# Optimization experiments

Hardware: AMD Instinct MI355X
Metric: run time of the kernel (lower is better)

Reference implementation:

```python
import jax, jax.numpy as jnp
from jax import lax
import numpy as np

OUT_CH = 64
K = 7
STRIDE = 2
PAD = 3
HIDDEN = 128
MAX_IN = 3


def setup_inputs() -> dict:
    key = jax.random.key(0)
    k1, k2, k3, k4, k5 = jax.random.split(key, 5)
    B, C, H, W = 32, MAX_IN, 224, 224
    x = jax.random.normal(k1, (B, C, H, W), dtype=jnp.float32)
    channel_mask = jnp.ones((B, C), dtype=jnp.float32)
    # kernel_generator params: Linear(3,128) -> ReLU -> Linear(128, 64*3*7*7)
    W1 = jax.random.normal(k2, (MAX_IN, HIDDEN), dtype=jnp.float32) / np.sqrt(MAX_IN)
    b1 = jnp.zeros((HIDDEN,), dtype=jnp.float32)
    out_dim = OUT_CH * MAX_IN * K * K
    W2 = jax.random.normal(k3, (HIDDEN, out_dim), dtype=jnp.float32) / np.sqrt(HIDDEN)
    b2 = jnp.zeros((out_dim,), dtype=jnp.float32)
    return {"x": x, "channel_mask": channel_mask, "W1": W1, "b1": b1, "W2": W2, "b2": b2}


def reference(x, channel_mask, W1, b1, W2, b2):
    B, C, H, W = x.shape
    # MLP kernel generator: [B, 3] -> [B, out*C*K*K]
    h = jax.nn.relu(channel_mask @ W1 + b1)
    weights = (h @ W2 + b2).reshape(B * OUT_CH, C, K, K)
    # grouped conv, groups = B (per-sample dynamic kernels)
    out = lax.conv_general_dilated(
        x.reshape(1, B * C, H, W),
        weights,
        window_strides=(STRIDE, STRIDE),
        padding=[(PAD, PAD), (PAD, PAD)],
        feature_group_count=B,
        dimension_numbers=("NCHW", "OIHW", "NCHW"),
    )
    return out.reshape(B, OUT_CH, out.shape[2], out.shape[3])
```

## Files before the change

### kernel.cpp

```cpp
#include <hip/hip_runtime.h>
#include <hip/hip_bf16.h>

#define OUT_CH 64
#define KSZ 7
#define STRIDE 2
#define PAD 3
#define HIDDEN 128
#define MAX_IN 3
#define B_SZ 32
#define H_IN 224
#define W_IN 224
#define H_OUT 112
#define W_OUT 112
#define WPB 147
#define OUT_DIM (OUT_CH * WPB)
#define SEGS 21
#define SEGP 24
#define WQ_PER_B (OUT_CH * SEGP * 8)
#define XRW 120
#define XSROWS 24
#define WGEN_BLOCKS 384
#define XPREP_BLOCKS 10080

typedef __attribute__((ext_vector_type(8))) short short8;
typedef __attribute__((ext_vector_type(4))) float floatx4;

__global__ void prep_kernel(const float* __restrict__ x,
                            const float* __restrict__ mask,
                            const float* __restrict__ W1,
                            const float* __restrict__ b1,
                            const float* __restrict__ W2,
                            const float* __restrict__ b2,
                            __hip_bfloat16* __restrict__ wq,
                            unsigned int* __restrict__ xbf,
                            unsigned int* __restrict__ zpad) {
    __shared__ float hs[4][HIDDEN];
    const int tid = threadIdx.x;
    const int bid = blockIdx.x;

    if (bid < WGEN_BLOCKS) {
        const int gb    = bid / 48;
        const int chunk = bid - gb * 48;
        const int b0 = gb * 4;

        for (int i = tid; i < 4 * HIDDEN; i += 256) {
            int q = i >> 7;
            int j = i & (HIDDEN - 1);
            float a = b1[j];
#pragma unroll
            for (int c = 0; c < MAX_IN; ++c)
                a += mask[(b0 + q) * MAX_IN + c] * W1[c * HIDDEN + j];
            hs[q][j] = fmaxf(a, 0.0f);
        }
        __syncthreads();

        const int op = chunk * 256 + tid;
        const int oc  = op / 192;
        const int r   = op - oc * 192;
        const int mi  = r >> 5;
        const int lg  = (r >> 3) & 3;
        const int e   = r & 7;
        const int seg = 4 * mi + 2 * (lg >> 1) + (e >> 2);
        const int tap = 4 * (lg & 1) + (e & 3);

        float acc[4] = {0.0f, 0.0f, 0.0f, 0.0f};
        if (seg < SEGS && tap < KSZ) {
            int o = oc * WPB + seg * KSZ + tap;
            float bias = b2[o];
#pragma unroll
            for (int q = 0; q < 4; ++q) acc[q] = bias;
            const float* w2p = W2 + o;
#pragma unroll 8
            for (int j = 0; j < HIDDEN; ++j) {
                float w = w2p[(size_t)j * OUT_DIM];
#pragma unroll
                for (int q = 0; q < 4; ++q) acc[q] += hs[q][j] * w;
            }
        }
#pragma unroll
        for (int q = 0; q < 4; ++q)
            wq[(size_t)(b0 + q) * WQ_PER_B + op] = __float2bfloat16(acc[q]);
    } else {
        const int xbid = bid - WGEN_BLOCKS;
        int s = xbid * 256 + tid;
        int r = s / XRW;
        int uw = s - r * XRW;
        const float* xr = x + (size_t)r * W_IN;
        int iw0 = 2 * uw - 3;
        float f0 = ((unsigned)iw0 < (unsigned)W_IN) ? xr[iw0] : 0.0f;
        float f1 = ((unsigned)(iw0 + 1) < (unsigned)W_IN) ? xr[iw0 + 1] : 0.0f;
        unsigned int lo = __bfloat16_as_ushort(__float2bfloat16(f0));
        unsigned int hi = __bfloat16_as_ushort(__float2bfloat16(f1));
        xbf[s] = lo | (hi << 16);
        if (xbid == 0 && tid < XRW) zpad[tid] = 0;
    }
}

__global__ void __launch_bounds__(256, 6)
conv_kernel(const unsigned int* __restrict__ xbf,
            const unsigned int* __restrict__ zpad,
            const __hip_bfloat16* __restrict__ wq,
            float* __restrict__ out) {
    __shared__ unsigned int xs[XSROWS * XRW];

    const int xblk = blockIdx.x;
    const int oh = (xblk & 7) * 14 + (xblk >> 3);
    const int b  = blockIdx.y;
    const int tid = threadIdx.x;
    const int w  = tid >> 6;
    const int l  = tid & 63;
    const int lr = l & 15;
    const int lg = l >> 4;

    const unsigned short* wqb = (const unsigned short*)wq
        + ((size_t)b * OUT_CH + w * 16 + lr) * (SEGP * 8);
    short8 afr[6];
#pragma unroll
    for (int mi = 0; mi < 6; ++mi)
        afr[mi] = *(const short8*)(wqb + mi * 32 + lg * 8);

    const int halfl = l / 30;
    const int lc    = l - 30 * halfl;
#pragma unroll
    for (int i = 0; i < 3; ++i) {
        int d   = w + 4 * i;
        int seg = 2 * d + halfl;
        const unsigned int* src = zpad;
        if (seg < SEGS) {
            int c  = seg / KSZ;
            int kh = seg - c * KSZ;
            int ih = oh * STRIDE + kh - PAD;
            if ((unsigned)ih < (unsigned)H_IN)
                src = xbf + ((size_t)(b * MAX_IN + c) * H_IN + ih) * XRW;
        }
        if (l < 60)
            __builtin_amdgcn_global_load_lds(
                (const __attribute__((address_space(1))) unsigned int*)(src + lc * 4),
                (__attribute__((address_space(3))) unsigned int*)(xs + d * 240),
                16, 0, 0);
    }
    __syncthreads();

    const int col = lr + 2 * (lg & 1);
    int ra[6], rb[6];
#pragma unroll
    for (int mi = 0; mi < 6; ++mi) {
        int sa = 4 * mi + 2 * (lg >> 1);
        int sb = sa + 1;
        ra[mi] = (sa < SEGS ? sa : 0) * XRW + col;
        rb[mi] = (sb < SEGS ? sb : 0) * XRW + col;
    }

#pragma unroll
    for (int t = 0; t < 7; ++t) {
        const int tb = t * 16;
        floatx4 acc = {0.0f, 0.0f, 0.0f, 0.0f};
#pragma unroll
        for (int mi = 0; mi < 6; ++mi) {
            union { short8 s; unsigned int u[4]; } bu;
            const unsigned int* pa = xs + ra[mi] + tb;
            const unsigned int* pb = xs + rb[mi] + tb;
            bu.u[0] = pa[0];
            bu.u[1] = pa[1];
            bu.u[2] = pb[0];
            bu.u[3] = pb[1];
            acc = __builtin_amdgcn_mfma_f32_16x16x32_bf16(afr[mi], bu.s, acc, 0, 0, 0);
        }
        const int ow = tb + lr;
        float* op = out + (((size_t)b * OUT_CH + w * 16 + lg * 4) * H_OUT + oh) * W_OUT + ow;
#pragma unroll
        for (int r = 0; r < 4; ++r)
            op[(size_t)r * H_OUT * W_OUT] = acc[r];
    }
}

extern "C" void kernel_launch(void* const* d_in, const int* in_sizes, int n_in,
                              void* d_out, int out_size, void* d_ws, size_t ws_size,
                              hipStream_t stream) {
    const float* x    = (const float*)d_in[0];
    const float* mask = (const float*)d_in[1];
    const float* W1   = (const float*)d_in[2];
    const float* b1   = (const float*)d_in[3];
    const float* W2   = (const float*)d_in[4];
    const float* b2   = (const float*)d_in[5];
    float* out = (float*)d_out;

    __hip_bfloat16* wq  = (__hip_bfloat16*)d_ws;
    unsigned int* xbf   = (unsigned int*)((char*)d_ws + 786432);
    unsigned int* zpad  = (unsigned int*)((char*)d_ws + 786432 + (size_t)B_SZ * MAX_IN * H_IN * XRW * 4);

    prep_kernel<<<dim3(WGEN_BLOCKS + XPREP_BLOCKS), dim3(256), 0, stream>>>(
        x, mask, W1, b1, W2, b2, wq, xbf, zpad);
    conv_kernel<<<dim3(112, B_SZ), dim3(256), 0, stream>>>(xbf, zpad, wq, out);
}
```

Measured before the change: 37.78 us.

## Have each conv wave compute two output-channel tiles over a split range of width tiles

The four waves are remapped so each computes two 16-channel output tiles over half of the seven width tiles, instead of one tile over all seven. Each LDS B-fragment read now feeds two MFMAs, roughly halving LDS traffic per MFMA, and the row-offset tables are replaced by one shared base address. In exchange each wave holds twice as many weight fragments in registers, and the occupancy hint drops from 6 to 4 blocks. The width split is uneven (4 tiles vs 3), so waves in a block may finish at different times.

```diff
diff --git a/kernel.cpp b/kernel.cpp
--- a/kernel.cpp
+++ b/kernel.cpp
@@ -96,7 +96,7 @@
     }
 }
 
-__global__ void __launch_bounds__(256, 6)
+__global__ void __launch_bounds__(256, 4)
 conv_kernel(const unsigned int* __restrict__ xbf,
             const unsigned int* __restrict__ zpad,
             const __hip_bfloat16* __restrict__ wq,
@@ -111,13 +111,23 @@
     const int l  = tid & 63;
     const int lr = l & 15;
     const int lg = l >> 4;
-
-    const unsigned short* wqb = (const unsigned short*)wq
-        + ((size_t)b * OUT_CH + w * 16 + lr) * (SEGP * 8);
-    short8 afr[6];
-#pragma unroll
-    for (int mi = 0; mi < 6; ++mi)
-        afr[mi] = *(const short8*)(wqb + mi * 32 + lg * 8);
+    const int ocp  = w >> 1;
+    const int tset = w & 1;
+
+    short8 afr[2][6];
+#pragma unroll
+    for (int q = 0; q < 2; ++q) {
+        const unsigned short* wqb = (const unsigned short*)wq
+            + ((size_t)b * OUT_CH + (2 * ocp + q) * 16 + lr) * (SEGP * 8);
+#pragma unroll
+        for (int mi = 0; mi < 6; ++mi)
+            afr[q][mi] = *(const short8*)(wqb + mi * 32 + lg * 8);
+    }
+#pragma unroll
+    for (int q = 0; q < 2; ++q)
+#pragma unroll
+        for (int mi = 0; mi < 6; ++mi)
+            asm volatile("" : "+v"(afr[q][mi]));
 
     const int halfl = l / 30;
     const int lc    = l - 30 * halfl;
@@ -142,35 +152,33 @@
     __syncthreads();
 
     const int col = lr + 2 * (lg & 1);
-    int ra[6], rb[6];
-#pragma unroll
-    for (int mi = 0; mi < 6; ++mi) {
-        int sa = 4 * mi + 2 * (lg >> 1);
-        int sb = sa + 1;
-        ra[mi] = (sa < SEGS ? sa : 0) * XRW + col;
-        rb[mi] = (sb < SEGS ? sb : 0) * XRW + col;
-    }
-
-#pragma unroll
-    for (int t = 0; t < 7; ++t) {
+    const int rbase = 2 * (lg >> 1) * XRW + col;
+
+    const int t0 = tset ? 4 : 0;
+    const int t1 = tset ? 7 : 4;
+    for (int t = t0; t < t1; ++t) {
         const int tb = t * 16;
-        floatx4 acc = {0.0f, 0.0f, 0.0f, 0.0f};
+        floatx4 acc0 = {0.0f, 0.0f, 0.0f, 0.0f};
+        floatx4 acc1 = {0.0f, 0.0f, 0.0f, 0.0f};
 #pragma unroll
         for (int mi = 0; mi < 6; ++mi) {
+            const unsigned int* pa = xs + (4 * mi) * XRW + rbase + tb;
             union { short8 s; unsigned int u[4]; } bu;
-            const unsigned int* pa = xs + ra[mi] + tb;
-            const unsigned int* pb = xs + rb[mi] + tb;
             bu.u[0] = pa[0];
             bu.u[1] = pa[1];
-            bu.u[2] = pb[0];
-            bu.u[3] = pb[1];
-            acc = __builtin_amdgcn_mfma_f32_16x16x32_bf16(afr[mi], bu.s, acc, 0, 0, 0);
+            bu.u[2] = pa[XRW];
+            bu.u[3] = pa[XRW + 1];
+            acc0 = __builtin_amdgcn_mfma_f32_16x16x32_bf16(afr[0][mi], bu.s, acc0, 0, 0, 0);
+            acc1 = __builtin_amdgcn_mfma_f32_16x16x32_bf16(afr[1][mi], bu.s, acc1, 0, 0, 0);
         }
         const int ow = tb + lr;
-        float* op = out + (((size_t)b * OUT_CH + w * 16 + lg * 4) * H_OUT + oh) * W_OUT + ow;
-#pragma unroll
-        for (int r = 0; r < 4; ++r)
-            op[(size_t)r * H_OUT * W_OUT] = acc[r];
+        float* op0 = out + (((size_t)b * OUT_CH + (2 * ocp) * 16 + lg * 4) * H_OUT + oh) * W_OUT + ow;
+        float* op1 = op0 + (size_t)16 * H_OUT * W_OUT;
+#pragma unroll
+        for (int r = 0; r < 4; ++r) {
+            op0[(size_t)r * H_OUT * W_OUT] = acc0[r];
+            op1[(size_t)r * H_OUT * W_OUT] = acc1[r];
+        }
     }
 }
 
```

Result: slower. 48.08 us (+27.3%).

## Compute two output rows per conv block to reuse overlapping input rows

Applied to the files above, without the earlier changes.

Each conv block now produces two adjacent output rows, loading 9 input rows per channel (27 plus a zero row) into shared memory instead of 7 per channel per output row. Overlapping rows are shared between the two outputs, and the per-batch weight fragments are loaded once for twice the work. This cuts redundant global-to-LDS input traffic and weight loads. In exchange the grid is halved to 56x32 blocks and each block uses more LDS, which lowers parallelism.

```diff
diff --git a/kernel.cpp b/kernel.cpp
--- a/kernel.cpp
+++ b/kernel.cpp
@@ -18,7 +18,8 @@
 #define SEGP 24
 #define WQ_PER_B (OUT_CH * SEGP * 8)
 #define XRW 120
-#define XSROWS 24
+#define XSROWS 28
+#define ZROW 27
 #define WGEN_BLOCKS 384
 #define XPREP_BLOCKS 10080
 
@@ -104,7 +105,8 @@
     __shared__ unsigned int xs[XSROWS * XRW];
 
     const int xblk = blockIdx.x;
-    const int oh = (xblk & 7) * 14 + (xblk >> 3);
+    const int ohp = (xblk & 7) * 7 + (xblk >> 3);
+    const int oh0 = ohp * 2;
     const int b  = blockIdx.y;
     const int tid = threadIdx.x;
     const int w  = tid >> 6;
@@ -122,14 +124,15 @@
     const int halfl = l / 30;
     const int lc    = l - 30 * halfl;
 #pragma unroll
-    for (int i = 0; i < 3; ++i) {
-        int d   = w + 4 * i;
-        int seg = 2 * d + halfl;
+    for (int i = 0; i < 4; ++i) {
+        int d = w + 4 * i;
+        if (d >= XSROWS / 2) break;
+        int row = 2 * d + halfl;
         const unsigned int* src = zpad;
-        if (seg < SEGS) {
-            int c  = seg / KSZ;
-            int kh = seg - c * KSZ;
-            int ih = oh * STRIDE + kh - PAD;
+        if (row < 27) {
+            int c = row / 9;
+            int j = row - c * 9;
+            int ih = 2 * oh0 + j - PAD;
             if ((unsigned)ih < (unsigned)H_IN)
                 src = xbf + ((size_t)(b * MAX_IN + c) * H_IN + ih) * XRW;
         }
@@ -142,35 +145,49 @@
     __syncthreads();
 
     const int col = lr + 2 * (lg & 1);
-    int ra[6], rb[6];
-#pragma unroll
-    for (int mi = 0; mi < 6; ++mi) {
-        int sa = 4 * mi + 2 * (lg >> 1);
-        int sb = sa + 1;
-        ra[mi] = (sa < SEGS ? sa : 0) * XRW + col;
-        rb[mi] = (sb < SEGS ? sb : 0) * XRW + col;
-    }
-
-#pragma unroll
-    for (int t = 0; t < 7; ++t) {
-        const int tb = t * 16;
-        floatx4 acc = {0.0f, 0.0f, 0.0f, 0.0f};
+
+#pragma unroll
+    for (int dh = 0; dh < 2; ++dh) {
+        const int oh = oh0 + dh;
+        int ra[6], rb[6];
 #pragma unroll
         for (int mi = 0; mi < 6; ++mi) {
-            union { short8 s; unsigned int u[4]; } bu;
-            const unsigned int* pa = xs + ra[mi] + tb;
-            const unsigned int* pb = xs + rb[mi] + tb;
-            bu.u[0] = pa[0];
-            bu.u[1] = pa[1];
-            bu.u[2] = pb[0];
-            bu.u[3] = pb[1];
-            acc = __builtin_amdgcn_mfma_f32_16x16x32_bf16(afr[mi], bu.s, acc, 0, 0, 0);
-        }
-        const int ow = tb + lr;
-        float* op = out + (((size_t)b * OUT_CH + w * 16 + lg * 4) * H_OUT + oh) * W_OUT + ow;
-#pragma unroll
-        for (int r = 0; r < 4; ++r)
-            op[(size_t)r * H_OUT * W_OUT] = acc[r];
+            int sa = 4 * mi + 2 * (lg >> 1);
+            int sb = sa + 1;
+            int rowa, rowb;
+            {
+                int c = sa / KSZ, kh = sa - c * KSZ;
+                rowa = (sa < SEGS) ? (c * 9 + kh + 2 * dh) : ZROW;
+            }
+            {
+                int c = sb / KSZ, kh = sb - c * KSZ;
+                rowb = (sb < SEGS) ? (c * 9 + kh + 2 * dh) : ZROW;
+            }
+            ra[mi] = rowa * XRW + col;
+            rb[mi] = rowb * XRW + col;
+        }
+
+#pragma unroll
+        for (int t = 0; t < 7; ++t) {
+            const int tb = t * 16;
+            floatx4 acc = {0.0f, 0.0f, 0.0f, 0.0f};
+#pragma unroll
+            for (int mi = 0; mi < 6; ++mi) {
+                union { short8 s; unsigned int u[4]; } bu;
+                const unsigned int* pa = xs + ra[mi] + tb;
+                const unsigned int* pb = xs + rb[mi] + tb;
+                bu.u[0] = pa[0];
+                bu.u[1] = pa[1];
+                bu.u[2] = pb[0];
+                bu.u[3] = pb[1];
+                acc = __builtin_amdgcn_mfma_f32_16x16x32_bf16(afr[mi], bu.s, acc, 0, 0, 0);
+            }
+            const int ow = tb + lr;
+            float* op = out + (((size_t)b * OUT_CH + w * 16 + lg * 4) * H_OUT + oh) * W_OUT + ow;
+#pragma unroll
+            for (int r = 0; r < 4; ++r)
+                op[(size_t)r * H_OUT * W_OUT] = acc[r];
+        }
     }
 }
 
@@ -191,5 +208,5 @@
 
     prep_kernel<<<dim3(WGEN_BLOCKS + XPREP_BLOCKS), dim3(256), 0, stream>>>(
         x, mask, W1, b1, W2, b2, wq, xbf, zpad);
-    conv_kernel<<<dim3(112, B_SZ), dim3(256), 0, stream>>>(xbf, zpad, wq, out);
+    conv_kernel<<<dim3(56, B_SZ), dim3(256), 0, stream>>>(xbf, zpad, wq, out);
 }
```

After: 38.02 us. Within noise of the previous version (+0.6%).
